# Kernel optimization log

Hardware: AMD Instinct MI355X
Metric: run time of the kernel (lower is better)

Reference implementation:

```python
import jax, jax.numpy as jnp
import numpy as np

EPS = 1e-6


def setup_inputs() -> dict:
    key = jax.random.key(0)
    k1, k2, k3 = jax.random.split(key, 3)
    B, N1, N2, D, K, C = 8, 1024, 1024, 1, 5, 3
    xa = jax.random.normal(k1, (B, N1, D, C), dtype=jnp.float32)
    features = jax.random.normal(k2, (B, N1, K, C), dtype=jnp.float32)
    xt = jax.random.normal(k3, (B, N2, D, C), dtype=jnp.float32)
    # learned parameter: log_std of shape (in_dims, num_basis, num_channels)
    log_std = jnp.log(1e-6 + 0.1 * jnp.ones((D, K, C), dtype=jnp.float32))
    return {"xa": xa, "features": features, "xt": xt, "log_std": log_std}


def reference(xa, features, xt, log_std):
    # xa: (B, N1, D, C), xt: (B, N2, D, C), features: (B, N1, K, C), log_std: (D, K, C)
    std = jnp.exp(log_std) + EPS                       # (D, K, C)
    x1 = xa[:, :, :, None, :] / std                    # (B, N1, D, K, C)
    x2 = xt[:, :, :, None, :] / std                    # (B, N2, D, K, C)
    sq1 = jnp.sum(x1 * x1, axis=2)                     # (B, N1, K, C)
    sq2 = jnp.sum(x2 * x2, axis=2)                     # (B, N2, K, C)
    # pairwise squared distance per basis/channel
    prod = jnp.einsum('bndkc,bmdkc->bnmkc', x1, x2)    # (B, N1, N2, K, C)
    dist = sq1[:, :, None] + sq2[:, None] - 2.0 * prod # (B, N1, N2, K, C)
    wt = jnp.exp(-0.5 * dist)                          # RBF weights
    # weighted sum over context points N1
    smoothed = jnp.einsum('bnkc,bnmkc->bmkc', features, wt)  # (B, N2, K, C)
    return smoothed
```

## Files before the change

kernel.cpp:

```cpp
#include <hip/hip_runtime.h>

#define EPS_F 1e-6f
#define LOG2E 1.4426950408889634f

typedef float f4a __attribute__((ext_vector_type(4), aligned(16)));

__global__ void icgp_coef_kernel(const float* __restrict__ log_std,
                                 float* __restrict__ cb) {
    if (threadIdx.x == 0) {
        float c[15];
        #pragma unroll
        for (int kc = 0; kc < 15; ++kc) {
            const float s = __expf(log_std[kc]) + EPS_F;
            c[kc] = -0.5f * LOG2E / (s * s);
        }
        bool uni = true;
        #pragma unroll
        for (int k = 1; k < 5; ++k)
            #pragma unroll
            for (int ch = 0; ch < 3; ++ch)
                uni = uni && (c[k * 3 + ch] == c[ch]);
        #pragma unroll
        for (int kc = 0; kc < 15; ++kc) cb[kc] = c[kc];
        cb[15] = uni ? 1.0f : 0.0f;
    }
}

__global__ __launch_bounds__(256, 4) void icgp_partial_kernel(
    const float* __restrict__ xa,
    const float* __restrict__ feat,
    const float* __restrict__ xt,
    const float* __restrict__ cb,
    float* __restrict__ pws)
{
    __shared__ float lds[3840];

    const int bid  = blockIdx.x;
    const int nc   = bid & 7;
    const int mt   = (bid >> 3) & 15;
    const int b    = bid >> 7;
    const int tid  = threadIdx.x;
    const int wv   = tid >> 6;
    const int lane = tid & 63;
    const int m    = mt * 64 + lane;

    float coef[15];
    #pragma unroll
    for (int kc = 0; kc < 15; ++kc) coef[kc] = cb[kc];
    const bool uni = (cb[15] != 0.0f);

    const float t0 = xt[(b * 1024 + m) * 3 + 0];
    const float t1 = xt[(b * 1024 + m) * 3 + 1];
    const float t2 = xt[(b * 1024 + m) * 3 + 2];

    const int rw = __builtin_amdgcn_readfirstlane(nc * 128 + wv * 32);
    const float* __restrict__ fg = feat + (size_t)b * 1024 * 15;
    const float* __restrict__ ag = xa   + (size_t)b * 1024 * 3;

    float acc[15];
    #pragma unroll
    for (int kc = 0; kc < 15; ++kc) acc[kc] = 0.0f;

    if (uni) {
        const float c0 = coef[0], c1 = coef[1], c2 = coef[2];
        #pragma unroll 4
        for (int i = 0; i < 32; ++i) {
            const int r = rw + i;
            const float* __restrict__ f = fg + r * 15;
            const float a0 = ag[r * 3 + 0];
            const float a1 = ag[r * 3 + 1];
            const float a2 = ag[r * 3 + 2];
            float d0 = a0 - t0; d0 *= d0;
            float d1 = a1 - t1; d1 *= d1;
            float d2 = a2 - t2; d2 *= d2;
            const float w0 = __builtin_amdgcn_exp2f(d0 * c0);
            const float w1 = __builtin_amdgcn_exp2f(d1 * c1);
            const float w2 = __builtin_amdgcn_exp2f(d2 * c2);
            acc[0]  += w0 * f[0];   acc[1]  += w1 * f[1];   acc[2]  += w2 * f[2];
            acc[3]  += w0 * f[3];   acc[4]  += w1 * f[4];   acc[5]  += w2 * f[5];
            acc[6]  += w0 * f[6];   acc[7]  += w1 * f[7];   acc[8]  += w2 * f[8];
            acc[9]  += w0 * f[9];   acc[10] += w1 * f[10];  acc[11] += w2 * f[11];
            acc[12] += w0 * f[12];  acc[13] += w1 * f[13];  acc[14] += w2 * f[14];
        }
    } else {
        for (int i = 0; i < 32; ++i) {
            const int r = rw + i;
            const float* __restrict__ f = fg + r * 15;
            const float a0 = ag[r * 3 + 0];
            const float a1 = ag[r * 3 + 1];
            const float a2 = ag[r * 3 + 2];
            float dd[3];
            dd[0] = a0 - t0; dd[0] *= dd[0];
            dd[1] = a1 - t1; dd[1] *= dd[1];
            dd[2] = a2 - t2; dd[2] *= dd[2];
            #pragma unroll
            for (int k = 0; k < 5; ++k)
                #pragma unroll
                for (int c = 0; c < 3; ++c)
                    acc[k * 3 + c] +=
                        __builtin_amdgcn_exp2f(dd[c] * coef[k * 3 + c]) * f[k * 3 + c];
        }
    }

    #pragma unroll
    for (int kc = 0; kc < 15; ++kc) lds[tid * 15 + kc] = acc[kc];
    __syncthreads();

    float* __restrict__ pb = pws + (size_t)nc * 122880
                                 + ((size_t)b * 1024 + mt * 64) * 15;
    #pragma unroll
    for (int j = 0; j < 4; ++j) {
        const int o = j * 256 + tid;
        if (o < 960) {
            const int mm = o / 15, kc = o - mm * 15;
            float s = 0.0f;
            #pragma unroll
            for (int w = 0; w < 4; ++w)
                s += lds[(w * 64 + mm) * 15 + kc];
            pb[o] = s;
        }
    }
}

__global__ __launch_bounds__(256) void icgp_reduce_kernel(
    const float* __restrict__ pws, float* __restrict__ out)
{
    const int idx = blockIdx.x * 256 + threadIdx.x;
    f4a s = {0.0f, 0.0f, 0.0f, 0.0f};
    #pragma unroll
    for (int ns = 0; ns < 8; ++ns) {
        const f4a v = *(const f4a*)(pws + (size_t)ns * 122880 + idx * 4);
        s.x += v.x; s.y += v.y; s.z += v.z; s.w += v.w;
    }
    *(f4a*)(out + idx * 4) = s;
}

extern "C" void kernel_launch(void* const* d_in, const int* in_sizes, int n_in,
                              void* d_out, int out_size, void* d_ws, size_t ws_size,
                              hipStream_t stream) {
    const float* xa      = (const float*)d_in[0];
    const float* feat    = (const float*)d_in[1];
    const float* xt      = (const float*)d_in[2];
    const float* log_std = (const float*)d_in[3];
    float* out = (float*)d_out;
    float* pws = (float*)d_ws;
    float* cb  = pws + 8 * 122880;

    icgp_coef_kernel<<<dim3(1), dim3(64), 0, stream>>>(log_std, cb);
    icgp_partial_kernel<<<dim3(1024), dim3(256), 0, stream>>>(xa, feat, xt, cb, pws);
    icgp_reduce_kernel<<<dim3(120), dim3(256), 0, stream>>>(pws, out);
}
```

Measured before the change: 74.29 us.

## Fuse split-N reduction into partial kernel via atomic last-block counter

```diff
diff --git a/kernel.cpp b/kernel.cpp
--- a/kernel.cpp
+++ b/kernel.cpp
@@ -5,8 +5,12 @@
 
 typedef float f4a __attribute__((ext_vector_type(4), aligned(16)));
 
+#define PWS_FLOATS (64 * 16 * 1920)
+
 __global__ void icgp_coef_kernel(const float* __restrict__ log_std,
-                                 float* __restrict__ cb) {
+                                 float* __restrict__ cb,
+                                 unsigned int* __restrict__ cnt) {
+    if (threadIdx.x < 64) cnt[threadIdx.x] = 0u;
     if (threadIdx.x == 0) {
         float c[15];
         #pragma unroll
@@ -31,108 +35,146 @@
     const float* __restrict__ feat,
     const float* __restrict__ xt,
     const float* __restrict__ cb,
-    float* __restrict__ pws)
+    float* __restrict__ pws,
+    unsigned int* __restrict__ cnt,
+    float* __restrict__ out)
 {
-    __shared__ float lds[3840];
+    __shared__ float lds[7680];
 
     const int bid  = blockIdx.x;
-    const int nc   = bid & 7;
-    const int mt   = (bid >> 3) & 15;
+    const int nc   = bid & 15;
+    const int mg   = (bid >> 4) & 7;
     const int b    = bid >> 7;
+    const int g    = b * 8 + mg;
     const int tid  = threadIdx.x;
     const int wv   = tid >> 6;
     const int lane = tid & 63;
-    const int m    = mt * 64 + lane;
 
     float coef[15];
     #pragma unroll
     for (int kc = 0; kc < 15; ++kc) coef[kc] = cb[kc];
     const bool uni = (cb[15] != 0.0f);
 
-    const float t0 = xt[(b * 1024 + m) * 3 + 0];
-    const float t1 = xt[(b * 1024 + m) * 3 + 1];
-    const float t2 = xt[(b * 1024 + m) * 3 + 2];
+    const int m0 = mg * 128 + lane;
+    const int m1 = m0 + 64;
+    const float t00 = xt[(b * 1024 + m0) * 3 + 0];
+    const float t01 = xt[(b * 1024 + m0) * 3 + 1];
+    const float t02 = xt[(b * 1024 + m0) * 3 + 2];
+    const float t10 = xt[(b * 1024 + m1) * 3 + 0];
+    const float t11 = xt[(b * 1024 + m1) * 3 + 1];
+    const float t12 = xt[(b * 1024 + m1) * 3 + 2];
 
-    const int rw = __builtin_amdgcn_readfirstlane(nc * 128 + wv * 32);
+    const int rw = __builtin_amdgcn_readfirstlane(nc * 64 + wv * 16);
     const float* __restrict__ fg = feat + (size_t)b * 1024 * 15;
     const float* __restrict__ ag = xa   + (size_t)b * 1024 * 3;
 
-    float acc[15];
+    float acc0[15], acc1[15];
     #pragma unroll
-    for (int kc = 0; kc < 15; ++kc) acc[kc] = 0.0f;
+    for (int kc = 0; kc < 15; ++kc) { acc0[kc] = 0.0f; acc1[kc] = 0.0f; }
 
     if (uni) {
         const float c0 = coef[0], c1 = coef[1], c2 = coef[2];
         #pragma unroll 4
-        for (int i = 0; i < 32; ++i) {
+        for (int i = 0; i < 16; ++i) {
             const int r = rw + i;
             const float* __restrict__ f = fg + r * 15;
             const float a0 = ag[r * 3 + 0];
             const float a1 = ag[r * 3 + 1];
             const float a2 = ag[r * 3 + 2];
-            float d0 = a0 - t0; d0 *= d0;
-            float d1 = a1 - t1; d1 *= d1;
-            float d2 = a2 - t2; d2 *= d2;
-            const float w0 = __builtin_amdgcn_exp2f(d0 * c0);
-            const float w1 = __builtin_amdgcn_exp2f(d1 * c1);
-            const float w2 = __builtin_amdgcn_exp2f(d2 * c2);
-            acc[0]  += w0 * f[0];   acc[1]  += w1 * f[1];   acc[2]  += w2 * f[2];
-            acc[3]  += w0 * f[3];   acc[4]  += w1 * f[4];   acc[5]  += w2 * f[5];
-            acc[6]  += w0 * f[6];   acc[7]  += w1 * f[7];   acc[8]  += w2 * f[8];
-            acc[9]  += w0 * f[9];   acc[10] += w1 * f[10];  acc[11] += w2 * f[11];
-            acc[12] += w0 * f[12];  acc[13] += w1 * f[13];  acc[14] += w2 * f[14];
+            float d0, d1, d2;
+            d0 = a0 - t00; d0 *= d0;
+            d1 = a1 - t01; d1 *= d1;
+            d2 = a2 - t02; d2 *= d2;
+            const float w00 = __builtin_amdgcn_exp2f(d0 * c0);
+            const float w01 = __builtin_amdgcn_exp2f(d1 * c1);
+            const float w02 = __builtin_amdgcn_exp2f(d2 * c2);
+            d0 = a0 - t10; d0 *= d0;
+            d1 = a1 - t11; d1 *= d1;
+            d2 = a2 - t12; d2 *= d2;
+            const float w10 = __builtin_amdgcn_exp2f(d0 * c0);
+            const float w11 = __builtin_amdgcn_exp2f(d1 * c1);
+            const float w12 = __builtin_amdgcn_exp2f(d2 * c2);
+            #pragma unroll
+            for (int k = 0; k < 5; ++k) {
+                acc0[k * 3 + 0] += w00 * f[k * 3 + 0];
+                acc0[k * 3 + 1] += w01 * f[k * 3 + 1];
+                acc0[k * 3 + 2] += w02 * f[k * 3 + 2];
+                acc1[k * 3 + 0] += w10 * f[k * 3 + 0];
+                acc1[k * 3 + 1] += w11 * f[k * 3 + 1];
+                acc1[k * 3 + 2] += w12 * f[k * 3 + 2];
+            }
         }
     } else {
-        for (int i = 0; i < 32; ++i) {
+        for (int i = 0; i < 16; ++i) {
             const int r = rw + i;
             const float* __restrict__ f = fg + r * 15;
             const float a0 = ag[r * 3 + 0];
             const float a1 = ag[r * 3 + 1];
             const float a2 = ag[r * 3 + 2];
-            float dd[3];
-            dd[0] = a0 - t0; dd[0] *= dd[0];
-            dd[1] = a1 - t1; dd[1] *= dd[1];
-            dd[2] = a2 - t2; dd[2] *= dd[2];
+            float dd0[3], dd1[3];
+            dd0[0] = a0 - t00; dd0[0] *= dd0[0];
+            dd0[1] = a1 - t01; dd0[1] *= dd0[1];
+            dd0[2] = a2 - t02; dd0[2] *= dd0[2];
+            dd1[0] = a0 - t10; dd1[0] *= dd1[0];
+            dd1[1] = a1 - t11; dd1[1] *= dd1[1];
+            dd1[2] = a2 - t12; dd1[2] *= dd1[2];
             #pragma unroll
             for (int k = 0; k < 5; ++k)
                 #pragma unroll
-                for (int c = 0; c < 3; ++c)
-                    acc[k * 3 + c] +=
-                        __builtin_amdgcn_exp2f(dd[c] * coef[k * 3 + c]) * f[k * 3 + c];
+                for (int c = 0; c < 3; ++c) {
+                    acc0[k * 3 + c] +=
+                        __builtin_amdgcn_exp2f(dd0[c] * coef[k * 3 + c]) * f[k * 3 + c];
+                    acc1[k * 3 + c] +=
+                        __builtin_amdgcn_exp2f(dd1[c] * coef[k * 3 + c]) * f[k * 3 + c];
+                }
         }
     }
 
     #pragma unroll
-    for (int kc = 0; kc < 15; ++kc) lds[tid * 15 + kc] = acc[kc];
+    for (int kc = 0; kc < 15; ++kc) {
+        lds[wv * 1920 + lane * 15 + kc]        = acc0[kc];
+        lds[wv * 1920 + (64 + lane) * 15 + kc] = acc1[kc];
+    }
     __syncthreads();
 
-    float* __restrict__ pb = pws + (size_t)nc * 122880
-                                 + ((size_t)b * 1024 + mt * 64) * 15;
+    float* __restrict__ pb = pws + ((size_t)g * 16 + nc) * 1920;
     #pragma unroll
-    for (int j = 0; j < 4; ++j) {
+    for (int j = 0; j < 8; ++j) {
         const int o = j * 256 + tid;
-        if (o < 960) {
-            const int mm = o / 15, kc = o - mm * 15;
+        if (o < 1920) {
             float s = 0.0f;
             #pragma unroll
             for (int w = 0; w < 4; ++w)
-                s += lds[(w * 64 + mm) * 15 + kc];
+                s += lds[w * 1920 + o];
             pb[o] = s;
         }
     }
-}
 
-__global__ __launch_bounds__(256) void icgp_reduce_kernel(
-    const float* __restrict__ pws, float* __restrict__ out)
-{
-    const int idx = blockIdx.x * 256 + threadIdx.x;
-    f4a s = {0.0f, 0.0f, 0.0f, 0.0f};
-    #pragma unroll
-    for (int ns = 0; ns < 8; ++ns) {
-        const f4a v = *(const f4a*)(pws + (size_t)ns * 122880 + idx * 4);
-        s.x += v.x; s.y += v.y; s.z += v.z; s.w += v.w;
+    __syncthreads();
+    __shared__ unsigned int last;
+    if (tid == 0) {
+        __threadfence();
+        last = atomicAdd(&cnt[g], 1u);
     }
-    *(f4a*)(out + idx * 4) = s;
+    __syncthreads();
+    if (last == 15u) {
+        __threadfence();
+        const float* __restrict__ rbase = pws + (size_t)g * 16 * 1920;
+        float* __restrict__ ob = out + ((size_t)b * 1024 + mg * 128) * 15;
+        #pragma unroll
+        for (int j = 0; j < 2; ++j) {
+            const int idx = j * 256 + tid;
+            if (idx < 480) {
+                f4a s = {0.0f, 0.0f, 0.0f, 0.0f};
+                #pragma unroll
+                for (int sl = 0; sl < 16; ++sl) {
+                    const f4a v = *(const f4a*)(rbase + sl * 1920 + idx * 4);
+                    s.x += v.x; s.y += v.y; s.z += v.z; s.w += v.w;
+                }
+                *(f4a*)(ob + idx * 4) = s;
+            }
+        }
+    }
 }
 
 extern "C" void kernel_launch(void* const* d_in, const int* in_sizes, int n_in,
@@ -144,9 +186,10 @@
     const float* log_std = (const float*)d_in[3];
     float* out = (float*)d_out;
     float* pws = (float*)d_ws;
-    float* cb  = pws + 8 * 122880;
+    float* cb  = pws + PWS_FLOATS;
+    unsigned int* cnt = (unsigned int*)(cb + 16);
 
-    icgp_coef_kernel<<<dim3(1), dim3(64), 0, stream>>>(log_std, cb);
-    icgp_partial_kernel<<<dim3(1024), dim3(256), 0, stream>>>(xa, feat, xt, cb, pws);
-    icgp_reduce_kernel<<<dim3(120), dim3(256), 0, stream>>>(pws, out);
+    icgp_coef_kernel<<<dim3(1), dim3(64), 0, stream>>>(log_std, cb, cnt);
+    icgp_partial_kernel<<<dim3(1024), dim3(256), 0, stream>>>(
+        xa, feat, xt, cb, pws, cnt, out);
 }
```

After: 125.6 us. 69.0% more time.
